# Kernel tuning notes

Hardware: AMD Instinct MI355X
Metric: run time of the kernel (lower is better)

## Reference

```python
import jax, jax.numpy as jnp
import numpy as np

E = 1024      # embedding_size
H = 16        # num_head
DQ = DK = DV = 64  # per-head q/k/v size


def setup_inputs() -> dict:
    key = jax.random.key(0)
    ks = jax.random.split(key, 9)
    B, S = 2, 2048
    s = 1.0 / np.sqrt(E)
    return {
        "q": jax.random.normal(ks[0], (B, S, E), jnp.float32),
        "k": jax.random.normal(ks[1], (B, S, E), jnp.float32),
        "v": jax.random.normal(ks[2], (B, S, E), jnp.float32),
        "w_q": jax.random.normal(ks[3], (E, H * DQ), jnp.float32) * s,
        "b_q": jax.random.normal(ks[4], (H * DQ,), jnp.float32) * s,
        "w_k": jax.random.normal(ks[5], (E, H * DK), jnp.float32) * s,
        "b_k": jax.random.normal(ks[6], (H * DK,), jnp.float32) * s,
        "w_v": jax.random.normal(ks[7], (E, H * DV), jnp.float32) * s,
        "b_v": jax.random.normal(ks[8], (H * DV,), jnp.float32) * s,
    }


def reference(q, k, v, w_q, b_q, w_k, b_k, w_v, b_v):
    B, Sq, _ = q.shape
    Sk = k.shape[1]
    # projections -> [B, S, H, d] -> [B, H, S, d]
    qh = (q @ w_q + b_q).reshape(B, Sq, H, DQ).transpose(0, 2, 1, 3)
    kh = (k @ w_k + b_k).reshape(B, Sk, H, DK).transpose(0, 2, 1, 3)
    vh = (v @ w_v + b_v).reshape(B, Sk, H, DV).transpose(0, 2, 1, 3)
    # scaled dot-product attention; scores [B, H, Sq, Sk]
    scores = jnp.einsum("bhqd,bhkd->bhqk", qh, kh) / jnp.sqrt(jnp.float32(DQ))
    weights = jax.nn.softmax(scores, axis=-1)
    out = jnp.einsum("bhqk,bhkd->bhqd", weights, vh)  # [B, H, Sq, DV]
    return out.transpose(0, 2, 1, 3).reshape(B, Sq, H * DV)
```

## Files before the change

### kernel.cpp

```cpp
#include <hip/hip_runtime.h>
#include <hip/hip_bf16.h>

typedef __bf16 bf16_t;
typedef bf16_t bf16x8 __attribute__((ext_vector_type(8)));
typedef bf16_t bf16x4 __attribute__((ext_vector_type(4)));
typedef short  short4v __attribute__((ext_vector_type(4)));
typedef float  f32x4  __attribute__((ext_vector_type(4)));

#define MFMA16(a,b,c) __builtin_amdgcn_mfma_f32_16x16x32_bf16(a, b, c, 0, 0, 0)

constexpr int S = 2048, H = 16, Dh = 64;
constexpr int N = H * Dh;
constexpr int K = 1024;
constexpr float QSCALE = 0.125f * 1.4426950408889634f;

static __device__ inline void load_lds16(const bf16_t* g, bf16_t* l) {
  __builtin_amdgcn_global_load_lds(
      (const __attribute__((address_space(1))) void*)g,
      (__attribute__((address_space(3))) void*)l, 16, 0, 0);
}

static __device__ inline ushort f2bb(float x) {
  bf16_t h = (bf16_t)x;
  return __builtin_bit_cast(ushort, h);
}

__global__ __launch_bounds__(256) void prep(
    const float* __restrict__ q, const float* __restrict__ k,
    const float* __restrict__ v,
    const float* __restrict__ wq, const float* __restrict__ wk,
    const float* __restrict__ wv,
    bf16_t* __restrict__ xq, bf16_t* __restrict__ xk, bf16_t* __restrict__ xv,
    bf16_t* __restrict__ wtq, bf16_t* __restrict__ wtk, bf16_t* __restrict__ wtv) {
  __shared__ ushort tile[64][68];
  int bx = blockIdx.x, t = threadIdx.x;
  if (bx < 6144) {
    int z = bx >> 11, bb = bx & 2047;
    const float* xi = z == 0 ? q : z == 1 ? k : v;
    bf16_t*      xo = z == 0 ? xq : z == 1 ? xk : xv;
    size_t idx = ((size_t)bb * 256 + t) * 8;
    float4 a = *(const float4*)&xi[idx];
    float4 b = *(const float4*)&xi[idx + 4];
    bf16x8 w;
    w[0] = (bf16_t)a.x; w[1] = (bf16_t)a.y; w[2] = (bf16_t)a.z; w[3] = (bf16_t)a.w;
    w[4] = (bf16_t)b.x; w[5] = (bf16_t)b.y; w[6] = (bf16_t)b.z; w[7] = (bf16_t)b.w;
    *(bf16x8*)&xo[idx] = w;
  } else {
    int zz = bx - 6144;
    int z = zz >> 8, bb = zz & 255;
    const float* wi = z == 0 ? wq : z == 1 ? wk : wv;
    ushort*      wo = (ushort*)(z == 0 ? wtq : z == 1 ? wtk : wtv);
    int k0 = (bb >> 4) * 64, n0 = (bb & 15) * 64;
    for (int i = 0; i < 4; ++i) {
      int idx4 = (i * 256 + t) * 4;
      int r = idx4 >> 6, c = idx4 & 63;
      float4 vv = *(const float4*)&wi[(size_t)(k0 + r) * N + n0 + c];
      tile[r][c] = f2bb(vv.x); tile[r][c + 1] = f2bb(vv.y);
      tile[r][c + 2] = f2bb(vv.z); tile[r][c + 3] = f2bb(vv.w);
    }
    __syncthreads();
    for (int i = 0; i < 4; ++i) {
      int idx4 = (i * 256 + t) * 4;
      int r = idx4 >> 6, c = idx4 & 63;
      ushort4 vv;
      vv.x = tile[c][r]; vv.y = tile[c + 1][r];
      vv.z = tile[c + 2][r]; vv.w = tile[c + 3][r];
      *(ushort4*)&wo[(size_t)(n0 + r) * K + k0 + c] = vv;
    }
  }
}

__global__ __launch_bounds__(256) void proj_gemm(
    const bf16_t* __restrict__ xq, const bf16_t* __restrict__ xk,
    const bf16_t* __restrict__ xv,
    const bf16_t* __restrict__ wtq, const bf16_t* __restrict__ wtk,
    const bf16_t* __restrict__ wtv,
    const float* __restrict__ bq, const float* __restrict__ bk,
    const float* __restrict__ bv,
    bf16_t* __restrict__ qh, bf16_t* __restrict__ kh, bf16_t* __restrict__ vt) {
  int bid = blockIdx.x;
  int logical = (bid & 7) * 96 + (bid >> 3);
  int mode = logical >> 8;
  int rem = logical & 255;
  int gx = rem & 7;
  int gy = rem >> 3;

  const bf16_t* X  = mode == 0 ? xq  : mode == 1 ? xk  : wtv;
  const bf16_t* Wt = mode == 0 ? wtq : mode == 1 ? wtk : xv;
  const float*  Bi = mode == 0 ? bq  : mode == 1 ? bk  : bv;

  __shared__ __align__(16) bf16_t smem[17408];
  bf16_t (*Ash)[64] = (bf16_t(*)[64])smem;
  bf16_t (*Bsh)[64] = (bf16_t(*)[64])(smem + 8192);
  bf16_t* Cs = smem;

  int tid = threadIdx.x;
  int wave = tid >> 6, lane = tid & 63;
  int lr = lane & 15, lg = lane >> 4;
  int lrow = lane >> 3, lchunk = lane & 7;
  int m0 = (mode < 2 ? gy : gx) * 128;
  int n0 = (mode < 2 ? gx : gy) * 128;
  int wm = (wave >> 1) * 64, wn = (wave & 1) * 64;

  f32x4 acc[4][4];
  for (int i = 0; i < 4; ++i)
    for (int j = 0; j < 4; ++j) acc[i][j] = (f32x4){0.f, 0.f, 0.f, 0.f};

  for (int ko = 0; ko < K / 64; ++ko) {
    __syncthreads();
    for (int j = 0; j < 4; ++j) {
      int r = wave * 32 + j * 8 + lrow;
      int gc = (lchunk ^ (r & 7)) * 8;
      load_lds16(&X [(size_t)(m0 + r) * K + ko * 64 + gc], &Ash[r][lchunk * 8]);
      load_lds16(&Wt[(size_t)(n0 + r) * K + ko * 64 + gc], &Bsh[r][lchunk * 8]);
    }
    __syncthreads();
    for (int kk = 0; kk < 2; ++kk) {
      bf16x8 af[4], bfr[4];
      for (int i = 0; i < 4; ++i) {
        int rr = wm + i * 16 + lr;
        af[i] = *(const bf16x8*)&Ash[rr][(((kk << 2) | lg) ^ (rr & 7)) * 8];
      }
      for (int j = 0; j < 4; ++j) {
        int rr = wn + j * 16 + lr;
        bfr[j] = *(const bf16x8*)&Bsh[rr][(((kk << 2) | lg) ^ (rr & 7)) * 8];
      }
      for (int i = 0; i < 4; ++i)
        for (int j = 0; j < 4; ++j)
          acc[i][j] = MFMA16(af[i], bfr[j], acc[i][j]);
    }
  }

  float badd[4][4][4];
  if (mode < 2) {
    float bvv[4];
    for (int j = 0; j < 4; ++j) bvv[j] = Bi[n0 + wn + j * 16 + lr];
    for (int i = 0; i < 4; ++i)
      for (int j = 0; j < 4; ++j)
        for (int r = 0; r < 4; ++r) badd[i][j][r] = bvv[j];
  } else {
    for (int i = 0; i < 4; ++i)
      for (int r = 0; r < 4; ++r) {
        float bm = Bi[m0 + wm + i * 16 + lg * 4 + r];
        for (int j = 0; j < 4; ++j) badd[i][j][r] = bm;
      }
  }

  __syncthreads();
  for (int i = 0; i < 4; ++i)
    for (int j = 0; j < 4; ++j)
      for (int r = 0; r < 4; ++r) {
        float vvv = acc[i][j][r] + badd[i][j][r];
        if (mode == 0) vvv *= QSCALE;
        Cs[(size_t)(wm + i * 16 + lg * 4 + r) * 136 + wn + j * 16 + lr] = (bf16_t)vvv;
      }
  __syncthreads();

  bf16_t* o = mode == 0 ? qh : mode == 1 ? kh : vt;
  for (int p = 0; p < 8; ++p) {
    int idx = p * 256 + tid;
    int row = idx >> 4, ch = idx & 15;
    bf16x8 vv = *(const bf16x8*)&Cs[(size_t)row * 136 + ch * 8];
    size_t dst;
    if (mode < 2) {
      int m_g = m0 + row, n_g = n0 + ch * 8;
      int b = m_g >> 11, s = m_g & 2047;
      int h = n_g >> 6, d = n_g & 63;
      dst = (((size_t)(b * 16 + h) * 2048) + s) * 64 + d;
    } else {
      int w_g = m0 + row, t_g = n0 + ch * 8;
      int b = t_g >> 11, s = t_g & 2047;
      dst = ((size_t)(b * 1024 + w_g)) * 2048 + s;
    }
    *(uint4*)&o[dst] = __builtin_bit_cast(uint4, vv);
  }
}

__global__ __launch_bounds__(512, 2) void attn(
    const bf16_t* __restrict__ qh, const bf16_t* __restrict__ kh,
    const bf16_t* __restrict__ vt, float* __restrict__ out) {
  __shared__ __align__(16) bf16_t smem[32768];

  int tid = threadIdx.x, wave = tid >> 6, lane = tid & 63;
  int lr = lane & 15, lg = lane >> 4;
  int half = wave >> 2, w4 = wave & 3;

  int bid = blockIdx.x;
  int logical = (bid & 7) * 64 + (bid >> 3);
  int bh = logical >> 4;
  int q0 = (logical & 15) * 128 + w4 * 32;

  bf16_t* kt0 = smem + half * 8192;

  const bf16_t* qg = qh + (size_t)bh * S * Dh;
  const bf16_t* kg = kh + (size_t)bh * S * Dh;
  const bf16_t* vg = vt + (size_t)bh * Dh * S;

  bf16x8 bqf[2][2];
#pragma unroll
  for (int ms = 0; ms < 2; ++ms)
#pragma unroll
    for (int kk = 0; kk < 2; ++kk)
      bqf[ms][kk] = *(const bf16x8*)
          &qg[(size_t)(q0 + ms * 16 + lr) * 64 + kk * 32 + lg * 8];

  bf16x8 ones8;
#pragma unroll
  for (int j = 0; j < 8; ++j) ones8[j] = (bf16_t)1.0f;

  f32x4 o_acc[2][4], lacc[2];
#pragma unroll
  for (int ms = 0; ms < 2; ++ms) {
    lacc[ms] = (f32x4){0.f, 0.f, 0.f, 0.f};
#pragma unroll
    for (int dt = 0; dt < 4; ++dt) o_acc[ms][dt] = (f32x4){0.f, 0.f, 0.f, 0.f};
  }

  int lrow = lane >> 3, lchunk = lane & 7;
  int srow0 = w4 * 16 + lrow;
  int srow1 = srow0 + 8;
  int sgc = (lchunk ^ (srow0 & 7)) * 8;
  int ld0 = srow0 * 64 + lchunk * 8;
  int ld1 = ld0 + 512;

  int cb = half * (S / 2);

  uint4 kr0 = *(const uint4*)&kg[(size_t)(cb + srow0) * 64 + sgc];
  uint4 kr1 = *(const uint4*)&kg[(size_t)(cb + srow1) * 64 + sgc];
  uint4 vr0 = *(const uint4*)&vg[(size_t)srow0 * S + cb + sgc];
  uint4 vr1 = *(const uint4*)&vg[(size_t)srow1 * S + cb + sgc];
  *(uint4*)&kt0[ld0] = kr0;
  *(uint4*)&kt0[ld1] = kr1;
  *(uint4*)&kt0[4096 + ld0] = vr0;
  *(uint4*)&kt0[4096 + ld1] = vr1;
  {
    int sk1 = cb + 64;
    kr0 = *(const uint4*)&kg[(size_t)(sk1 + srow0) * 64 + sgc];
    kr1 = *(const uint4*)&kg[(size_t)(sk1 + srow1) * 64 + sgc];
    vr0 = *(const uint4*)&vg[(size_t)srow0 * S + sk1 + sgc];
    vr1 = *(const uint4*)&vg[(size_t)srow1 * S + sk1 + sgc];
  }

  int sw = lr & 7, p4 = (lg & 1) * 4;

  constexpr int NITH = (S / 2) / 64;
  for (int it = 0; it < NITH; ++it) {
    __syncthreads();
    if (it + 1 < NITH) {
      int wb = ((it + 1) & 1) * 16384;
      *(uint4*)&kt0[wb + ld0] = kr0;
      *(uint4*)&kt0[wb + ld1] = kr1;
      *(uint4*)&kt0[wb + 4096 + ld0] = vr0;
      *(uint4*)&kt0[wb + 4096 + ld1] = vr1;
      if (it + 2 < NITH) {
        int sk = cb + (it + 2) * 64;
        kr0 = *(const uint4*)&kg[(size_t)(sk + srow0) * 64 + sgc];
        kr1 = *(const uint4*)&kg[(size_t)(sk + srow1) * 64 + sgc];
        vr0 = *(const uint4*)&vg[(size_t)srow0 * S + sk + sgc];
        vr1 = *(const uint4*)&vg[(size_t)srow1 * S + sk + sgc];
      }
    }
    const bf16_t* ktr = kt0 + (it & 1) * 16384;
    const bf16_t* vsr = ktr + 4096;

    bf16x8 pa8[2][2];
#pragma unroll
    for (int tp = 0; tp < 2; ++tp) {
      f32x4 st[2][2];
#pragma unroll
      for (int ms = 0; ms < 2; ++ms)
#pragma unroll
        for (int ts = 0; ts < 2; ++ts) st[ms][ts] = (f32x4){0.f, 0.f, 0.f, 0.f};
#pragma unroll
      for (int ts = 0; ts < 2; ++ts) {
        int t = tp * 2 + ts;
        const bf16_t* krow = &ktr[(t * 16 + lr) * 64];
        bf16x8 ak0 = *(const bf16x8*)&krow[(lg ^ sw) * 8];
        bf16x8 ak1 = *(const bf16x8*)&krow[((4 + lg) ^ sw) * 8];
#pragma unroll
        for (int ms = 0; ms < 2; ++ms) {
          st[ms][ts] = MFMA16(ak0, bqf[ms][0], st[ms][ts]);
          st[ms][ts] = MFMA16(ak1, bqf[ms][1], st[ms][ts]);
        }
      }
#pragma unroll
      for (int ms = 0; ms < 2; ++ms)
#pragma unroll
        for (int r = 0; r < 4; ++r) {
          pa8[ms][tp][r]     = (bf16_t)__builtin_amdgcn_exp2f(st[ms][0][r]);
          pa8[ms][tp][r + 4] = (bf16_t)__builtin_amdgcn_exp2f(st[ms][1][r]);
        }
    }

#pragma unroll
    for (int tp = 0; tp < 2; ++tp) {
      int g0 = tp * 4 + (lg >> 1);
#pragma unroll
      for (int dt = 0; dt < 4; ++dt) {
        const bf16_t* vrow = &vsr[(dt * 16 + lr) * 64];
        bf16x4 lo = *(const bf16x4*)&vrow[((g0      ^ sw) * 8) + p4];
        bf16x4 hi = *(const bf16x4*)&vrow[(((g0 + 2) ^ sw) * 8) + p4];
        bf16x8 bb;
#pragma unroll
        for (int j = 0; j < 4; ++j) { bb[j] = lo[j]; bb[j + 4] = hi[j]; }
#pragma unroll
        for (int ms = 0; ms < 2; ++ms)
          o_acc[ms][dt] = MFMA16(pa8[ms][tp], bb, o_acc[ms][dt]);
      }
#pragma unroll
      for (int ms = 0; ms < 2; ++ms)
        lacc[ms] = MFMA16(pa8[ms][tp], ones8, lacc[ms]);
    }
  }

  __syncthreads();
  float* mo = (float*)smem;
  float* ls = mo + 8 * 16 * 64;

  if (half == 1) {
#pragma unroll
    for (int ms = 0; ms < 2; ++ms)
#pragma unroll
      for (int r = 0; r < 4; ++r) {
        int row = (w4 * 2 + ms) * 16 + lg * 4 + r;
#pragma unroll
        for (int dt = 0; dt < 4; ++dt)
          mo[row * 64 + dt * 16 + lr] = o_acc[ms][dt][r];
        if (lr == 0) ls[row] = lacc[ms][r];
      }
  }
  __syncthreads();
  if (half == 0) {
    int b = bh >> 4, hh = bh & 15;
#pragma unroll
    for (int ms = 0; ms < 2; ++ms)
#pragma unroll
      for (int r = 0; r < 4; ++r) {
        int row = (w4 * 2 + ms) * 16 + lg * 4 + r;
        float inv = 1.f / (lacc[ms][r] + ls[row]);
        int s_row = q0 + ms * 16 + lg * 4 + r;
        size_t base = ((size_t)(b * S + s_row)) * 1024 + hh * 64;
#pragma unroll
        for (int dt = 0; dt < 4; ++dt)
          out[base + dt * 16 + lr] =
              (o_acc[ms][dt][r] + mo[row * 64 + dt * 16 + lr]) * inv;
      }
  }
}

extern "C" void kernel_launch(void* const* d_in, const int* in_sizes, int n_in,
                              void* d_out, int out_size, void* d_ws, size_t ws_size,
                              hipStream_t stream) {
  const float* q  = (const float*)d_in[0];
  const float* k  = (const float*)d_in[1];
  const float* v  = (const float*)d_in[2];
  const float* wq = (const float*)d_in[3];
  const float* bq = (const float*)d_in[4];
  const float* wk = (const float*)d_in[5];
  const float* bk = (const float*)d_in[6];
  const float* wv = (const float*)d_in[7];
  const float* bv = (const float*)d_in[8];

  bf16_t* ws  = (bf16_t*)d_ws;
  constexpr size_t MW = (size_t)1 << 20;
  constexpr size_t MX = (size_t)4096 * 1024;
  bf16_t* wtq = ws;
  bf16_t* wtk = wtq + MW;
  bf16_t* wtv = wtk + MW;
  bf16_t* xq  = wtv + MW;
  bf16_t* xk  = xq + MX;
  bf16_t* xv  = xk + MX;
  bf16_t* qhd = xv + MX;
  bf16_t* khd = qhd + MX;
  bf16_t* vtd = khd + MX;
  float* out  = (float*)d_out;

  prep<<<6912, 256, 0, stream>>>(q, k, v, wq, wk, wv,
                                 xq, xk, xv, wtq, wtk, wtv);
  proj_gemm<<<768, 256, 0, stream>>>(xq, xk, xv, wtq, wtk, wtv,
                                     bq, bk, bv, qhd, khd, vtd);
  attn<<<512, 512, 0, stream>>>(qhd, khd, vtd, out);
}
```

Baseline: 196.9 us.

## Load K fragments directly from global memory instead of staging through LDS

K tiles are no longer staged in shared memory. Each wave now reads its K MFMA fragments straight from global memory at the start of every iteration, and only V stays double-buffered in LDS, which shrinks the shared allocation. This removes the LDS writes and reads for K and lowers LDS pressure. In exchange, each of the four waves per half re-reads the same K rows from global or cache, and the loads sit on the critical path with no software prefetch ahead of the barrier.

```diff
diff --git a/kernel.cpp b/kernel.cpp
--- a/kernel.cpp
+++ b/kernel.cpp
@@ -179,7 +179,7 @@
 __global__ __launch_bounds__(512, 2) void attn(
     const bf16_t* __restrict__ qh, const bf16_t* __restrict__ kh,
     const bf16_t* __restrict__ vt, float* __restrict__ out) {
-  __shared__ __align__(16) bf16_t smem[32768];
+  __shared__ __align__(16) bf16_t smem[16640];
 
   int tid = threadIdx.x, wave = tid >> 6, lane = tid & 63;
   int lr = lane & 15, lg = lane >> 4;
@@ -190,7 +190,7 @@
   int bh = logical >> 4;
   int q0 = (logical & 15) * 128 + w4 * 32;
 
-  bf16_t* kt0 = smem + half * 8192;
+  bf16_t* vb = smem + half * 4096;
 
   const bf16_t* qg = qh + (size_t)bh * S * Dh;
   const bf16_t* kg = kh + (size_t)bh * S * Dh;
@@ -225,18 +225,12 @@
 
   int cb = half * (S / 2);
 
-  uint4 kr0 = *(const uint4*)&kg[(size_t)(cb + srow0) * 64 + sgc];
-  uint4 kr1 = *(const uint4*)&kg[(size_t)(cb + srow1) * 64 + sgc];
   uint4 vr0 = *(const uint4*)&vg[(size_t)srow0 * S + cb + sgc];
   uint4 vr1 = *(const uint4*)&vg[(size_t)srow1 * S + cb + sgc];
-  *(uint4*)&kt0[ld0] = kr0;
-  *(uint4*)&kt0[ld1] = kr1;
-  *(uint4*)&kt0[4096 + ld0] = vr0;
-  *(uint4*)&kt0[4096 + ld1] = vr1;
+  *(uint4*)&vb[ld0] = vr0;
+  *(uint4*)&vb[ld1] = vr1;
   {
     int sk1 = cb + 64;
-    kr0 = *(const uint4*)&kg[(size_t)(sk1 + srow0) * 64 + sgc];
-    kr1 = *(const uint4*)&kg[(size_t)(sk1 + srow1) * 64 + sgc];
     vr0 = *(const uint4*)&vg[(size_t)srow0 * S + sk1 + sgc];
     vr1 = *(const uint4*)&vg[(size_t)srow1 * S + sk1 + sgc];
   }
@@ -245,23 +239,26 @@
 
   constexpr int NITH = (S / 2) / 64;
   for (int it = 0; it < NITH; ++it) {
+    bf16x8 ak[4][2];
+#pragma unroll
+    for (int t = 0; t < 4; ++t)
+#pragma unroll
+      for (int kk = 0; kk < 2; ++kk)
+        ak[t][kk] = *(const bf16x8*)
+            &kg[(size_t)(cb + it * 64 + t * 16 + lr) * 64 + kk * 32 + lg * 8];
+
     __syncthreads();
     if (it + 1 < NITH) {
-      int wb = ((it + 1) & 1) * 16384;
-      *(uint4*)&kt0[wb + ld0] = kr0;
-      *(uint4*)&kt0[wb + ld1] = kr1;
-      *(uint4*)&kt0[wb + 4096 + ld0] = vr0;
-      *(uint4*)&kt0[wb + 4096 + ld1] = vr1;
+      bf16_t* w = vb + ((it + 1) & 1) * 8192;
+      *(uint4*)&w[ld0] = vr0;
+      *(uint4*)&w[ld1] = vr1;
       if (it + 2 < NITH) {
         int sk = cb + (it + 2) * 64;
-        kr0 = *(const uint4*)&kg[(size_t)(sk + srow0) * 64 + sgc];
-        kr1 = *(const uint4*)&kg[(size_t)(sk + srow1) * 64 + sgc];
         vr0 = *(const uint4*)&vg[(size_t)srow0 * S + sk + sgc];
         vr1 = *(const uint4*)&vg[(size_t)srow1 * S + sk + sgc];
       }
     }
-    const bf16_t* ktr = kt0 + (it & 1) * 16384;
-    const bf16_t* vsr = ktr + 4096;
+    const bf16_t* vsr = vb + (it & 1) * 8192;
 
     bf16x8 pa8[2][2];
 #pragma unroll
@@ -274,13 +271,10 @@
 #pragma unroll
       for (int ts = 0; ts < 2; ++ts) {
         int t = tp * 2 + ts;
-        const bf16_t* krow = &ktr[(t * 16 + lr) * 64];
-        bf16x8 ak0 = *(const bf16x8*)&krow[(lg ^ sw) * 8];
-        bf16x8 ak1 = *(const bf16x8*)&krow[((4 + lg) ^ sw) * 8];
 #pragma unroll
         for (int ms = 0; ms < 2; ++ms) {
-          st[ms][ts] = MFMA16(ak0, bqf[ms][0], st[ms][ts]);
-          st[ms][ts] = MFMA16(ak1, bqf[ms][1], st[ms][ts]);
+          st[ms][ts] = MFMA16(ak[t][0], bqf[ms][0], st[ms][ts]);
+          st[ms][ts] = MFMA16(ak[t][1], bqf[ms][1], st[ms][ts]);
         }
       }
 #pragma unroll
```

Measured after the change: 218.4 us. 10.9% more time.

## Fuse activation fp32-to-bf16 conversion into projection GEMM tile loads

Applied to the files above, without the earlier changes.

Removes the separate prep pass that converted q/k/v from fp32 to bf16 in workspace. The projection GEMM now reads fp32 activations directly, with a one-step register prefetch, and converts them to bf16 before writing them to LDS. The weight side still uses the direct global-to-LDS DMA path. This drops a full write and re-read of the bf16 activation copies, but the GEMM now reads twice as many bytes per activation tile, adds conversion work and register pressure, and loses async DMA for that operand.

```diff
diff --git a/kernel.cpp b/kernel.cpp
--- a/kernel.cpp
+++ b/kernel.cpp
@@ -26,53 +26,36 @@
 }
 
 __global__ __launch_bounds__(256) void prep(
-    const float* __restrict__ q, const float* __restrict__ k,
-    const float* __restrict__ v,
     const float* __restrict__ wq, const float* __restrict__ wk,
     const float* __restrict__ wv,
-    bf16_t* __restrict__ xq, bf16_t* __restrict__ xk, bf16_t* __restrict__ xv,
     bf16_t* __restrict__ wtq, bf16_t* __restrict__ wtk, bf16_t* __restrict__ wtv) {
   __shared__ ushort tile[64][68];
   int bx = blockIdx.x, t = threadIdx.x;
-  if (bx < 6144) {
-    int z = bx >> 11, bb = bx & 2047;
-    const float* xi = z == 0 ? q : z == 1 ? k : v;
-    bf16_t*      xo = z == 0 ? xq : z == 1 ? xk : xv;
-    size_t idx = ((size_t)bb * 256 + t) * 8;
-    float4 a = *(const float4*)&xi[idx];
-    float4 b = *(const float4*)&xi[idx + 4];
-    bf16x8 w;
-    w[0] = (bf16_t)a.x; w[1] = (bf16_t)a.y; w[2] = (bf16_t)a.z; w[3] = (bf16_t)a.w;
-    w[4] = (bf16_t)b.x; w[5] = (bf16_t)b.y; w[6] = (bf16_t)b.z; w[7] = (bf16_t)b.w;
-    *(bf16x8*)&xo[idx] = w;
-  } else {
-    int zz = bx - 6144;
-    int z = zz >> 8, bb = zz & 255;
-    const float* wi = z == 0 ? wq : z == 1 ? wk : wv;
-    ushort*      wo = (ushort*)(z == 0 ? wtq : z == 1 ? wtk : wtv);
-    int k0 = (bb >> 4) * 64, n0 = (bb & 15) * 64;
-    for (int i = 0; i < 4; ++i) {
-      int idx4 = (i * 256 + t) * 4;
-      int r = idx4 >> 6, c = idx4 & 63;
-      float4 vv = *(const float4*)&wi[(size_t)(k0 + r) * N + n0 + c];
-      tile[r][c] = f2bb(vv.x); tile[r][c + 1] = f2bb(vv.y);
-      tile[r][c + 2] = f2bb(vv.z); tile[r][c + 3] = f2bb(vv.w);
-    }
-    __syncthreads();
-    for (int i = 0; i < 4; ++i) {
-      int idx4 = (i * 256 + t) * 4;
-      int r = idx4 >> 6, c = idx4 & 63;
-      ushort4 vv;
-      vv.x = tile[c][r]; vv.y = tile[c + 1][r];
-      vv.z = tile[c + 2][r]; vv.w = tile[c + 3][r];
-      *(ushort4*)&wo[(size_t)(n0 + r) * K + k0 + c] = vv;
-    }
+  int z = bx >> 8, bb = bx & 255;
+  const float* wi = z == 0 ? wq : z == 1 ? wk : wv;
+  ushort*      wo = (ushort*)(z == 0 ? wtq : z == 1 ? wtk : wtv);
+  int k0 = (bb >> 4) * 64, n0 = (bb & 15) * 64;
+  for (int i = 0; i < 4; ++i) {
+    int idx4 = (i * 256 + t) * 4;
+    int r = idx4 >> 6, c = idx4 & 63;
+    float4 vv = *(const float4*)&wi[(size_t)(k0 + r) * N + n0 + c];
+    tile[r][c] = f2bb(vv.x); tile[r][c + 1] = f2bb(vv.y);
+    tile[r][c + 2] = f2bb(vv.z); tile[r][c + 3] = f2bb(vv.w);
+  }
+  __syncthreads();
+  for (int i = 0; i < 4; ++i) {
+    int idx4 = (i * 256 + t) * 4;
+    int r = idx4 >> 6, c = idx4 & 63;
+    ushort4 vv;
+    vv.x = tile[c][r]; vv.y = tile[c + 1][r];
+    vv.z = tile[c + 2][r]; vv.w = tile[c + 3][r];
+    *(ushort4*)&wo[(size_t)(n0 + r) * K + k0 + c] = vv;
   }
 }
 
 __global__ __launch_bounds__(256) void proj_gemm(
-    const bf16_t* __restrict__ xq, const bf16_t* __restrict__ xk,
-    const bf16_t* __restrict__ xv,
+    const float* __restrict__ qf, const float* __restrict__ kf,
+    const float* __restrict__ vf,
     const bf16_t* __restrict__ wtq, const bf16_t* __restrict__ wtk,
     const bf16_t* __restrict__ wtv,
     const float* __restrict__ bq, const float* __restrict__ bk,
@@ -85,8 +68,8 @@
   int gx = rem & 7;
   int gy = rem >> 3;
 
-  const bf16_t* X  = mode == 0 ? xq  : mode == 1 ? xk  : wtv;
-  const bf16_t* Wt = mode == 0 ? wtq : mode == 1 ? wtk : xv;
+  const float*  Cf = mode == 0 ? qf  : mode == 1 ? kf  : vf;
+  const bf16_t* Dm = mode == 0 ? wtq : mode == 1 ? wtk : wtv;
   const float*  Bi = mode == 0 ? bq  : mode == 1 ? bk  : bv;
 
   __shared__ __align__(16) bf16_t smem[17408];
@@ -102,17 +85,49 @@
   int n0 = (mode < 2 ? gx : gy) * 128;
   int wm = (wave >> 1) * 64, wn = (wave & 1) * 64;
 
+  int cvt_base = mode < 2 ? m0 : n0;
+  int dma_base = mode < 2 ? n0 : m0;
+  bf16_t (*CvtSh)[64] = mode < 2 ? Ash : Bsh;
+  bf16_t (*DmaSh)[64] = mode < 2 ? Bsh : Ash;
+
   f32x4 acc[4][4];
   for (int i = 0; i < 4; ++i)
     for (int j = 0; j < 4; ++j) acc[i][j] = (f32x4){0.f, 0.f, 0.f, 0.f};
 
+  float4 pfa[4], pfb[4];
+#pragma unroll
+  for (int j = 0; j < 4; ++j) {
+    int r = wave * 32 + j * 8 + lrow;
+    int gc = (lchunk ^ (r & 7)) * 8;
+    const float* s = &Cf[(size_t)(cvt_base + r) * K + gc];
+    pfa[j] = *(const float4*)s;
+    pfb[j] = *(const float4*)(s + 4);
+  }
+
   for (int ko = 0; ko < K / 64; ++ko) {
     __syncthreads();
+#pragma unroll
     for (int j = 0; j < 4; ++j) {
       int r = wave * 32 + j * 8 + lrow;
       int gc = (lchunk ^ (r & 7)) * 8;
-      load_lds16(&X [(size_t)(m0 + r) * K + ko * 64 + gc], &Ash[r][lchunk * 8]);
-      load_lds16(&Wt[(size_t)(n0 + r) * K + ko * 64 + gc], &Bsh[r][lchunk * 8]);
+      bf16x8 w;
+      w[0] = (bf16_t)pfa[j].x; w[1] = (bf16_t)pfa[j].y;
+      w[2] = (bf16_t)pfa[j].z; w[3] = (bf16_t)pfa[j].w;
+      w[4] = (bf16_t)pfb[j].x; w[5] = (bf16_t)pfb[j].y;
+      w[6] = (bf16_t)pfb[j].z; w[7] = (bf16_t)pfb[j].w;
+      *(bf16x8*)&CvtSh[r][lchunk * 8] = w;
+      load_lds16(&Dm[(size_t)(dma_base + r) * K + ko * 64 + gc],
+                 &DmaSh[r][lchunk * 8]);
+    }
+    if (ko + 1 < K / 64) {
+#pragma unroll
+      for (int j = 0; j < 4; ++j) {
+        int r = wave * 32 + j * 8 + lrow;
+        int gc = (lchunk ^ (r & 7)) * 8;
+        const float* s = &Cf[(size_t)(cvt_base + r) * K + (ko + 1) * 64 + gc];
+        pfa[j] = *(const float4*)s;
+        pfb[j] = *(const float4*)(s + 4);
+      }
     }
     __syncthreads();
     for (int kk = 0; kk < 2; ++kk) {
@@ -367,17 +382,13 @@
   bf16_t* wtq = ws;
   bf16_t* wtk = wtq + MW;
   bf16_t* wtv = wtk + MW;
-  bf16_t* xq  = wtv + MW;
-  bf16_t* xk  = xq + MX;
-  bf16_t* xv  = xk + MX;
-  bf16_t* qhd = xv + MX;
+  bf16_t* qhd = wtv + MW;
   bf16_t* khd = qhd + MX;
   bf16_t* vtd = khd + MX;
   float* out  = (float*)d_out;
 
-  prep<<<6912, 256, 0, stream>>>(q, k, v, wq, wk, wv,
-                                 xq, xk, xv, wtq, wtk, wtv);
-  proj_gemm<<<768, 256, 0, stream>>>(xq, xk, xv, wtq, wtk, wtv,
+  prep<<<768, 256, 0, stream>>>(wq, wk, wv, wtq, wtk, wtv);
+  proj_gemm<<<768, 256, 0, stream>>>(q, k, v, wtq, wtk, wtv,
                                      bq, bk, bv, qhd, khd, vtd);
   attn<<<512, 512, 0, stream>>>(qhd, khd, vtd, out);
 }
```

Result: slower. 203.6 us (+3.4%).
